# Performance work log

Hardware: AMD Instinct MI355X
Metric: run time of the kernel (lower is better)

Reference implementation:

```python
import jax, jax.numpy as jnp
import numpy as np


def setup_inputs() -> dict:
    key = jax.random.key(0)
    ks = jax.random.split(key, 10)
    B, C, D, H, W = 2, 512, 8, 32, 32
    Ck = C // 4  # shared KV head dim (and fixed query dim per intended MQA math)
    s = 0.02
    return {
        "x": jax.random.normal(ks[0], (B, C, D, H, W), dtype=jnp.float32),
        "Wq": jax.random.normal(ks[1], (Ck, C), dtype=jnp.float32) * s,
        "bq": jnp.zeros((Ck,), dtype=jnp.float32),
        "Wk": jax.random.normal(ks[2], (Ck, C), dtype=jnp.float32) * s,
        "bk": jnp.zeros((Ck,), dtype=jnp.float32),
        "Wv": jax.random.normal(ks[3], (Ck, C), dtype=jnp.float32) * s,
        "bv": jnp.zeros((Ck,), dtype=jnp.float32),
        "Wo": jax.random.normal(ks[4], (C, C), dtype=jnp.float32) * s,
        "bo": jnp.zeros((C,), dtype=jnp.float32),
    }


def reference(x, Wq, bq, Wk, bk, Wv, bv, Wo, bo):
    B, C, D, H, W = x.shape
    N = D * H * W
    Ck = Wk.shape[0]  # C // 4
    xf = x.reshape(B, C, N)  # flatten spatial dims -> sequence axis
    # 1x1 Conv3d == per-voxel linear projection over channels
    q = jnp.einsum('oc,bcn->bno', Wq, xf) + bq  # [B, N, Ck]
    k = jnp.einsum('oc,bcn->bno', Wk, xf) + bk  # [B, N, Ck]
    v = jnp.einsum('oc,bcn->bno', Wv, xf) + bv  # [B, N, Ck]
    scale = jnp.asarray(Ck, x.dtype) ** -0.5
    attn = jax.nn.softmax(jnp.einsum('bnc,bmc->bnm', q, k) * scale, axis=-1)  # [B, N, N]
    out = jnp.einsum('bnm,bmc->bnc', attn, v)  # [B, N, Ck]
    out = jnp.tile(out, (1, 1, 4))  # repeat(1,1,4) -> [B, N, C]
    out = jnp.einsum('oc,bnc->bon', Wo, out) + bo[None, :, None]  # [B, C, N]
    return out.reshape(B, C, D, H, W) + x
```

## Files before the change

kernel.cpp:

```cpp
#include <hip/hip_runtime.h>
#include <hip/hip_bf16.h>

typedef __bf16 bf16;
typedef __bf16 bf16x8 __attribute__((ext_vector_type(8)));
typedef __bf16 bf16x4 __attribute__((ext_vector_type(4)));
typedef float  f32x4  __attribute__((ext_vector_type(4)));
typedef float  f32x16 __attribute__((ext_vector_type(16)));
typedef unsigned int u32;
typedef u32 u32x4 __attribute__((ext_vector_type(4)));

constexpr int BB = 2, C = 512, NN = 8192, CK = 128;

__device__ __forceinline__ u32 cvt_pk_bf16(float lo, float hi) {
    u32 r;
    asm("v_cvt_pk_bf16_f32 %0, %1, %2" : "=v"(r) : "v"(lo), "v"(hi));
    return r;
}
__device__ __forceinline__ void pl32_swap(u32& a, u32& b) {
    asm("v_permlane32_swap_b32 %0, %1" : "+v"(a), "+v"(b));
}

__global__ __launch_bounds__(256) void k_qkv(
    const float* __restrict__ x,
    const float* __restrict__ Wq, const float* __restrict__ bq,
    const float* __restrict__ Wk, const float* __restrict__ bk,
    const float* __restrict__ Wv, const float* __restrict__ bv,
    bf16* __restrict__ qkv_ws)
{
    const int t = threadIdx.x;
    const int lane = t & 63, w = t >> 6;
    const int lr = lane & 15, lg = lane >> 4;
    const int n0 = blockIdx.x * 128;
    const int which = blockIdx.y;
    const int b = blockIdx.z;
    const float* W    = which == 0 ? Wq : (which == 1 ? Wk : Wv);
    const float* bias = which == 0 ? bq : (which == 1 ? bk : bv);
    bf16* out = qkv_ws + (size_t)which * BB * NN * CK;

    __shared__ __align__(16) char s_xT[128 * 144];
    __shared__ __align__(16) char s_w [128 * 144];

    f32x4 acc[2][8];
#pragma unroll
    for (int m = 0; m < 2; m++)
#pragma unroll
        for (int j = 0; j < 8; j++) acc[m][j] = (f32x4){0.f, 0.f, 0.f, 0.f};

    const float* xb = x + (size_t)b * C * NN;

    const int tok4 = (t & 31) * 4;
    const int c8   = (t >> 5) * 8;
    const int ob   = t >> 2;
    const int c16  = (t & 3) * 16;

    for (int kt = 0; kt < C; kt += 64) {
        __syncthreads();
        {
            float4 v[8];
#pragma unroll
            for (int i = 0; i < 8; i++)
                v[i] = *(const float4*)(xb + (size_t)(kt + c8 + i) * NN + n0 + tok4);
#pragma unroll
            for (int j = 0; j < 4; j++) {
                int tok = tok4 + j;
                bf16x8 pk = { (bf16)v[0].x, (bf16)v[1].x, (bf16)v[2].x, (bf16)v[3].x,
                              (bf16)v[4].x, (bf16)v[5].x, (bf16)v[6].x, (bf16)v[7].x };
                if (j == 1) pk = (bf16x8){ (bf16)v[0].y, (bf16)v[1].y, (bf16)v[2].y, (bf16)v[3].y,
                                           (bf16)v[4].y, (bf16)v[5].y, (bf16)v[6].y, (bf16)v[7].y };
                if (j == 2) pk = (bf16x8){ (bf16)v[0].z, (bf16)v[1].z, (bf16)v[2].z, (bf16)v[3].z,
                                           (bf16)v[4].z, (bf16)v[5].z, (bf16)v[6].z, (bf16)v[7].z };
                if (j == 3) pk = (bf16x8){ (bf16)v[0].w, (bf16)v[1].w, (bf16)v[2].w, (bf16)v[3].w,
                                           (bf16)v[4].w, (bf16)v[5].w, (bf16)v[6].w, (bf16)v[7].w };
                int off = tok * 144 + ((c8 * 2) ^ ((((tok >> 2) & 7)) << 4));
                *(bf16x8*)(s_xT + off) = pk;
            }
        }
#pragma unroll
        for (int p = 0; p < 2; p++) {
            int o = ob + p * 64;
            const float* wp = W + (size_t)o * C + kt + c16;
            float4 a0 = *(const float4*)(wp);
            float4 a1 = *(const float4*)(wp + 4);
            float4 a2 = *(const float4*)(wp + 8);
            float4 a3 = *(const float4*)(wp + 12);
            bf16x8 p0 = { (bf16)a0.x, (bf16)a0.y, (bf16)a0.z, (bf16)a0.w,
                          (bf16)a1.x, (bf16)a1.y, (bf16)a1.z, (bf16)a1.w };
            bf16x8 p1 = { (bf16)a2.x, (bf16)a2.y, (bf16)a2.z, (bf16)a2.w,
                          (bf16)a3.x, (bf16)a3.y, (bf16)a3.z, (bf16)a3.w };
            int perm = ((o >> 2) & 7) << 4;
            *(bf16x8*)(s_w + o * 144 + ((c16 * 2) ^ perm)) = p0;
            *(bf16x8*)(s_w + o * 144 + ((c16 * 2 + 16) ^ perm)) = p1;
        }
        __syncthreads();
#pragma unroll
        for (int ks = 0; ks < 2; ks++) {
            bf16x8 af[2];
#pragma unroll
            for (int m = 0; m < 2; m++) {
                int row = w * 32 + m * 16 + lr;
                af[m] = *(const bf16x8*)(s_xT + row * 144 + ((ks * 64 + lg * 16) ^ ((((row >> 2) & 7)) << 4)));
            }
#pragma unroll
            for (int j = 0; j < 8; j++) {
                int row = j * 16 + lr;
                bf16x8 bfr = *(const bf16x8*)(s_w + row * 144 + ((ks * 64 + lg * 16) ^ ((((row >> 2) & 7)) << 4)));
                acc[0][j] = __builtin_amdgcn_mfma_f32_16x16x32_bf16(af[0], bfr, acc[0][j], 0, 0, 0);
                acc[1][j] = __builtin_amdgcn_mfma_f32_16x16x32_bf16(af[1], bfr, acc[1][j], 0, 0, 0);
            }
        }
    }
#pragma unroll
    for (int m = 0; m < 2; m++)
#pragma unroll
        for (int j = 0; j < 8; j++) {
            int o = j * 16 + lr;
            float bia = bias[o];
#pragma unroll
            for (int r = 0; r < 4; r++) {
                int tok = n0 + w * 32 + m * 16 + lg * 4 + r;
                out[((size_t)b * NN + tok) * CK + o] = (bf16)(acc[m][j][r] + bia);
            }
        }
}

__global__ __launch_bounds__(512, 2) void k_attn(
    const bf16* __restrict__ qkv_ws,
    float* __restrict__ Opart, float* __restrict__ Lw,
    int nsplit)
{
    const int t = threadIdx.x;
    const int lane = t & 63, w = t >> 6;
    const int lq = lane & 31, hi = lane >> 5;

    const int total = 32 * BB * nsplit;
    const int chunkv = total >> 3;
    const int lin = blockIdx.x;
    const int rid = (lin & 7) * chunkv + (lin >> 3);
    const int qt = rid & 31;
    const int bs = rid >> 5;
    const int b = bs & 1, split = bs >> 1;

    const int q0 = qt * 256;
    const int kbeg = split * (NN / nsplit);
    const int nt = (NN / nsplit) / 64;

    const bf16* kg = qkv_ws + (size_t)BB * NN * CK;
    const bf16* vg = qkv_ws + (size_t)2 * BB * NN * CK;

    __shared__ __align__(16) char s_k[2][64 * 256];
    __shared__ __align__(16) char s_vt[3][128 * 128];

    const int kb0 = lq * 256 + ((((lq & 7) ^ hi)) << 4);
    int vbs[4];
#pragma unroll
    for (int db = 0; db < 4; db++) {
        int d = db * 32 + lq;
        vbs[db] = d * 128 + (((((d ^ (d >> 3)) & 7) ^ hi)) << 4);
    }
    const int t2 = t & 255;
    const int sc = t2 & 15, sr = t2 >> 4;
    const int kw_base = (sr * 256 + sc * 16) ^ ((sr & 7) << 4);
    const int vw_base = (sc * 1024 + sr * 8) ^ ((sc & 7) << 4);

    bf16x8 qf[8];
    {
        const float qs = 0.08838834764831845f * 1.4426950408889634f;
        const bf16* qp = qkv_ws + ((size_t)b * NN + q0 + w * 32 + lq) * CK + hi * 8;
#pragma unroll
        for (int ks = 0; ks < 8; ks++) {
            bf16x8 v = *(const bf16x8*)(qp + ks * 16);
#pragma unroll
            for (int i = 0; i < 8; i++) qf[ks][i] = (bf16)((float)v[i] * qs);
        }
    }

    f32x16 oacc[4];
#pragma unroll
    for (int db = 0; db < 4; db++)
#pragma unroll
        for (int i = 0; i < 16; i++) oacc[db][i] = 0.f;
    float lrun = 0.f;

    const bf16* kp = kg + ((size_t)b * NN + kbeg + sr) * CK + sc * 8;
    const bf16* vp = vg + ((size_t)b * NN + kbeg + sr * 4) * CK + sc * 8;
    bf16x8 stg[4];

    auto issue_loads = [&]() {
        if (w < 4) {
#pragma unroll
            for (int p = 0; p < 4; p++) stg[p] = *(const bf16x8*)(kp + (size_t)(16 * p) * CK);
        } else {
#pragma unroll
            for (int p = 0; p < 4; p++) stg[p] = *(const bf16x8*)(vp + (size_t)p * CK);
        }
        kp += (size_t)64 * CK;
        vp += (size_t)64 * CK;
    };

    auto write_lds = [&](int kbuf, int vbuf) {
        if (w < 4) {
            char* skw = s_k[kbuf] + kw_base;
#pragma unroll
            for (int p = 0; p < 4; p++)
                *(bf16x8*)(skw + p * 4096) = stg[p];
        } else {
            char* svw = s_vt[vbuf];
#pragma unroll
            for (int i = 0; i < 8; i++) {
                bf16x4 pk = { stg[0][i], stg[1][i], stg[2][i], stg[3][i] };
                *(bf16x4*)(svw + (vw_base ^ (i * 144))) = pk;
            }
        }
    };

    f32x16 sa0, sa1;
    auto do_qkt = [&](const char* sk) {
#pragma unroll
        for (int i = 0; i < 16; i++) { sa0[i] = 0.f; sa1[i] = 0.f; }
#pragma unroll
        for (int ks = 0; ks < 8; ks++) {
            bf16x8 kf0 = *(const bf16x8*)(sk + (kb0 ^ (ks * 32)));
            bf16x8 kf1 = *(const bf16x8*)(sk + ((kb0 ^ (ks * 32)) + 8192));
            sa0 = __builtin_amdgcn_mfma_f32_32x32x16_bf16(kf0, qf[ks], sa0, 0, 0, 0);
            sa1 = __builtin_amdgcn_mfma_f32_32x32x16_bf16(kf1, qf[ks], sa1, 0, 0, 0);
        }
    };

    u32 W0[8], W1[8];
    auto do_softmax = [&]() {
        f32x16 p0, p1;
#pragma unroll
        for (int i = 0; i < 16; i++) { p0[i] = exp2f(sa0[i]); p1[i] = exp2f(sa1[i]); }
        float s0 = ((p0[0] + p0[1]) + (p0[2] + p0[3])) + ((p0[4] + p0[5]) + (p0[6] + p0[7]));
        float s1 = ((p0[8] + p0[9]) + (p0[10] + p0[11])) + ((p0[12] + p0[13]) + (p0[14] + p0[15]));
        float s2 = ((p1[0] + p1[1]) + (p1[2] + p1[3])) + ((p1[4] + p1[5]) + (p1[6] + p1[7]));
        float s3 = ((p1[8] + p1[9]) + (p1[10] + p1[11])) + ((p1[12] + p1[13]) + (p1[14] + p1[15]));
        lrun += (s0 + s1) + (s2 + s3);
#pragma unroll
        for (int j = 0; j < 8; j++) {
            W0[j] = cvt_pk_bf16(p0[2 * j], p0[2 * j + 1]);
            W1[j] = cvt_pk_bf16(p1[2 * j], p1[2 * j + 1]);
        }
        pl32_swap(W0[0], W0[2]); pl32_swap(W0[1], W0[3]);
        pl32_swap(W0[4], W0[6]); pl32_swap(W0[5], W0[7]);
        pl32_swap(W1[0], W1[2]); pl32_swap(W1[1], W1[3]);
        pl32_swap(W1[4], W1[6]); pl32_swap(W1[5], W1[7]);
    };

    auto do_pv = [&](const char* sv) {
#pragma unroll
        for (int s = 0; s < 4; s++) {
            u32x4 fw;
            if (s == 0)      fw = (u32x4){W0[0], W0[1], W0[2], W0[3]};
            else if (s == 1) fw = (u32x4){W0[4], W0[5], W0[6], W0[7]};
            else if (s == 2) fw = (u32x4){W1[0], W1[1], W1[2], W1[3]};
            else             fw = (u32x4){W1[4], W1[5], W1[6], W1[7]};
            bf16x8 pa = __builtin_bit_cast(bf16x8, fw);
            const int coff = (s >> 1) * 64 + (s & 1) * 32;
#pragma unroll
            for (int db = 0; db < 4; db++) {
                bf16x8 vf = *(const bf16x8*)(sv + (vbs[db] ^ coff));
                oacc[db] = __builtin_amdgcn_mfma_f32_32x32x16_bf16(pa, vf, oacc[db], 0, 0, 0);
            }
        }
    };

    issue_loads();
    write_lds(0, 0);
    __syncthreads();
    if (nt > 1) issue_loads();
    __builtin_amdgcn_s_setprio(1);
    do_qkt(s_k[0]);
    __builtin_amdgcn_s_setprio(0);
    do_softmax();

    int vb_w = 1, vb_r = 0;
    for (int it = 1; it < nt; it++) {
        write_lds(it & 1, vb_w);
        __syncthreads();
        if (it + 1 < nt) issue_loads();
        __builtin_amdgcn_s_setprio(1);
        do_qkt(s_k[it & 1]);
        do_pv(s_vt[vb_r]);
        __builtin_amdgcn_s_setprio(0);
        do_softmax();
        vb_r = vb_w;
        vb_w = vb_w + 1 == 3 ? 0 : vb_w + 1;
    }
    __builtin_amdgcn_s_setprio(1);
    do_pv(s_vt[vb_r]);
    __builtin_amdgcn_s_setprio(0);

    size_t obase = (((size_t)split * BB + b) * NN + q0 + w * 32);
    float ls = lrun + __shfl_xor(lrun, 32);
    if (lane < 32) {
        Lw[obase + lq] = ls;
    }
#pragma unroll
    for (int r = 0; r < 16; r++) {
        int qrow = (r & 3) + 8 * (r >> 2) + 4 * hi;
        float* op = Opart + (obase + qrow) * CK + lq;
#pragma unroll
        for (int db = 0; db < 4; db++) op[db * 32] = oacc[db][r];
    }
}

__global__ __launch_bounds__(256) void k_combine(
    const float* __restrict__ Opart, const float* __restrict__ Lw,
    bf16* __restrict__ ao, int nsplit)
{
    const int t = threadIdx.x;
    const int b = blockIdx.y;
    const int r0 = blockIdx.x * 64;
    const int d4 = (t & 31) * 4;
#pragma unroll
    for (int p = 0; p < 8; p++) {
        int row = r0 + (t >> 5) + p * 8;
        size_t rbase = (size_t)b * NN + row;
        float L = 0.f;
        float4 acc = {0.f, 0.f, 0.f, 0.f};
        for (int s = 0; s < nsplit; s++) {
            size_t sb = ((size_t)s * BB) * NN + rbase;
            L += Lw[sb];
            float4 v = *(const float4*)(Opart + sb * CK + d4);
            acc.x += v.x; acc.y += v.y;
            acc.z += v.z; acc.w += v.w;
        }
        float inv = 1.f / L;
        bf16x4 o4 = { (bf16)(acc.x * inv), (bf16)(acc.y * inv),
                      (bf16)(acc.z * inv), (bf16)(acc.w * inv) };
        *(bf16x4*)(ao + rbase * CK + d4) = o4;
    }
}

__global__ __launch_bounds__(256) void k_out(
    const float* __restrict__ x, const float* __restrict__ Wo, const float* __restrict__ bo,
    const bf16* __restrict__ ao, float* __restrict__ y)
{
    const int t = threadIdx.x;
    const int lane = t & 63, w = t >> 6;
    const int lr = lane & 15, lg = lane >> 4;
    const int n0 = blockIdx.x * 128;
    const int o0 = blockIdx.y * 64;
    const int b = blockIdx.z;

    __shared__ __align__(16) char s_w[64 * 256];
    __shared__ __align__(16) char s_a[128 * 256];

    {
        int c4 = (t & 31) * 4, rbase = t >> 5;
#pragma unroll
        for (int p = 0; p < 8; p++) {
            int row = rbase + p * 8;
            const float* wp = Wo + (size_t)(o0 + row) * C + c4;
            float4 a0 = *(const float4*)(wp);
            float4 a1 = *(const float4*)(wp + 128);
            float4 a2 = *(const float4*)(wp + 256);
            float4 a3 = *(const float4*)(wp + 384);
            bf16x4 r4 = { (bf16)(a0.x + a1.x + a2.x + a3.x), (bf16)(a0.y + a1.y + a2.y + a3.y),
                          (bf16)(a0.z + a1.z + a2.z + a3.z), (bf16)(a0.w + a1.w + a2.w + a3.w) };
            int off = (row * 256 + c4 * 2) ^ ((row & 7) << 4);
            *(bf16x4*)(s_w + off) = r4;
        }
    }
    {
        int chunk = t & 15, rbase = t >> 4;
#pragma unroll
        for (int p = 0; p < 8; p++) {
            int row = rbase + p * 16;
            bf16x8 v = *(const bf16x8*)(ao + ((size_t)b * NN + n0 + row) * CK + chunk * 8);
            int off = (row * 256 + chunk * 16) ^ ((row & 7) << 4);
            *(bf16x8*)(s_a + off) = v;
        }
    }
    __syncthreads();

    f32x4 acc[8];
#pragma unroll
    for (int j = 0; j < 8; j++) acc[j] = (f32x4){0.f, 0.f, 0.f, 0.f};
#pragma unroll
    for (int ks = 0; ks < 4; ks++) {
        int row = w * 16 + lr;
        int aoff = (row * 256 + (ks * 32 + lg * 8) * 2) ^ ((row & 7) << 4);
        bf16x8 wf = *(const bf16x8*)(s_w + aoff);
#pragma unroll
        for (int j = 0; j < 8; j++) {
            int nrow = j * 16 + lr;
            int boff = (nrow * 256 + (ks * 32 + lg * 8) * 2) ^ ((nrow & 7) << 4);
            bf16x8 af = *(const bf16x8*)(s_a + boff);
            acc[j] = __builtin_amdgcn_mfma_f32_16x16x32_bf16(wf, af, acc[j], 0, 0, 0);
        }
    }
#pragma unroll
    for (int j = 0; j < 8; j++) {
        int n = n0 + j * 16 + lr;
#pragma unroll
        for (int r = 0; r < 4; r++) {
            int o = o0 + w * 16 + lg * 4 + r;
            size_t idx = ((size_t)b * C + o) * NN + n;
            y[idx] = acc[j][r] + bo[o] + x[idx];
        }
    }
}

extern "C" void kernel_launch(void* const* d_in, const int* in_sizes, int n_in,
                              void* d_out, int out_size, void* d_ws, size_t ws_size,
                              hipStream_t stream)
{
    const float* x  = (const float*)d_in[0];
    const float* Wq = (const float*)d_in[1];
    const float* bq = (const float*)d_in[2];
    const float* Wk = (const float*)d_in[3];
    const float* bk = (const float*)d_in[4];
    const float* Wv = (const float*)d_in[5];
    const float* bv = (const float*)d_in[6];
    const float* Wo = (const float*)d_in[7];
    const float* bo = (const float*)d_in[8];
    float* y = (float*)d_out;

    const size_t qkv_elems = (size_t)3 * BB * NN * CK;
    const size_t ao_elems  = (size_t)BB * NN * CK;

    bf16* qkv = (bf16*)d_ws;
    bf16* ao  = qkv + qkv_elems;
    float* Opart = (float*)(ao + ao_elems);

    int nsplit = 4;
    {
        size_t fixed = (qkv_elems + ao_elems) * sizeof(bf16);
        size_t per_split = ((size_t)BB * NN * CK + (size_t)BB * NN) * sizeof(float);
        while (nsplit > 1 && fixed + (size_t)nsplit * per_split > ws_size) nsplit >>= 1;
    }
    float* Lw = Opart + (size_t)nsplit * BB * NN * CK;

    k_qkv<<<dim3(NN / 128, 3, BB), 256, 0, stream>>>(x, Wq, bq, Wk, bk, Wv, bv, qkv);
    k_attn<<<dim3(32 * BB * nsplit, 1, 1), 512, 0, stream>>>(qkv, Opart, Lw, nsplit);
    k_combine<<<dim3(NN / 64, BB), 256, 0, stream>>>(Opart, Lw, ao, nsplit);
    k_out<<<dim3(NN / 128, C / 64, BB), 256, 0, stream>>>(x, Wo, bo, ao, y);
}
```

Baseline: 145.5 us.

## Enlarge attention blocks to 1024 threads, raise KV split, remap QKV grid

```diff
diff --git a/kernel.cpp b/kernel.cpp
--- a/kernel.cpp
+++ b/kernel.cpp
@@ -30,9 +30,14 @@
     const int t = threadIdx.x;
     const int lane = t & 63, w = t >> 6;
     const int lr = lane & 15, lg = lane >> 4;
-    const int n0 = blockIdx.x * 128;
-    const int which = blockIdx.y;
-    const int b = blockIdx.z;
+
+    const int lin = blockIdx.x;
+    const int rid = (lin & 7) * 48 + (lin >> 3);
+    const int n0 = (rid / 6) * 128;
+    const int sub = rid % 6;
+    const int which = sub >> 1;
+    const int b = sub & 1;
+
     const float* W    = which == 0 ? Wq : (which == 1 ? Wk : Wv);
     const float* bias = which == 0 ? bq : (which == 1 ? bk : bv);
     bf16* out = qkv_ws + (size_t)which * BB * NN * CK;
@@ -123,7 +128,7 @@
         }
 }
 
-__global__ __launch_bounds__(512, 2) void k_attn(
+__global__ __launch_bounds__(1024, 4) void k_attn(
     const bf16* __restrict__ qkv_ws,
     float* __restrict__ Opart, float* __restrict__ Lw,
     int nsplit)
@@ -132,15 +137,15 @@
     const int lane = t & 63, w = t >> 6;
     const int lq = lane & 31, hi = lane >> 5;
 
-    const int total = 32 * BB * nsplit;
+    const int total = 16 * BB * nsplit;
     const int chunkv = total >> 3;
     const int lin = blockIdx.x;
     const int rid = (lin & 7) * chunkv + (lin >> 3);
-    const int qt = rid & 31;
-    const int bs = rid >> 5;
+    const int qt = rid & 15;
+    const int bs = rid >> 4;
     const int b = bs & 1, split = bs >> 1;
 
-    const int q0 = qt * 256;
+    const int q0 = qt * 512;
     const int kbeg = split * (NN / nsplit);
     const int nt = (NN / nsplit) / 64;
 
@@ -157,10 +162,16 @@
         int d = db * 32 + lq;
         vbs[db] = d * 128 + (((((d ^ (d >> 3)) & 7) ^ hi)) << 4);
     }
-    const int t2 = t & 255;
-    const int sc = t2 & 15, sr = t2 >> 4;
-    const int kw_base = (sr * 256 + sc * 16) ^ ((sr & 7) << 4);
-    const int vw_base = (sc * 1024 + sr * 8) ^ ((sc & 7) << 4);
+    const int t2 = t & 511;
+    const int sck = t2 & 15, srk = t2 >> 4;
+    const int kw_base = (srk * 256 + sck * 16) ^ ((srk & 7) << 4);
+    const int sc4 = t2 & 31, sr4 = t2 >> 5;
+    int vw_addr[4];
+#pragma unroll
+    for (int i = 0; i < 4; i++) {
+        int d = sc4 * 4 + i;
+        vw_addr[i] = d * 128 + ((sr4 * 8) ^ (((d ^ (d >> 3)) & 7) << 4));
+    }
 
     bf16x8 qf[8];
     {
@@ -181,34 +192,35 @@
         for (int i = 0; i < 16; i++) oacc[db][i] = 0.f;
     float lrun = 0.f;
 
-    const bf16* kp = kg + ((size_t)b * NN + kbeg + sr) * CK + sc * 8;
-    const bf16* vp = vg + ((size_t)b * NN + kbeg + sr * 4) * CK + sc * 8;
-    bf16x8 stg[4];
+    const bf16* kp = kg + ((size_t)b * NN + kbeg + srk) * CK + sck * 8;
+    const bf16* vp = vg + ((size_t)b * NN + kbeg + sr4 * 4) * CK + sc4 * 4;
+    bf16x8 stgK[2];
+    bf16x4 stgV[4];
 
     auto issue_loads = [&]() {
-        if (w < 4) {
-#pragma unroll
-            for (int p = 0; p < 4; p++) stg[p] = *(const bf16x8*)(kp + (size_t)(16 * p) * CK);
+        if (w < 8) {
+#pragma unroll
+            for (int p = 0; p < 2; p++) stgK[p] = *(const bf16x8*)(kp + (size_t)(32 * p) * CK);
         } else {
 #pragma unroll
-            for (int p = 0; p < 4; p++) stg[p] = *(const bf16x8*)(vp + (size_t)p * CK);
+            for (int p = 0; p < 4; p++) stgV[p] = *(const bf16x4*)(vp + (size_t)p * CK);
         }
         kp += (size_t)64 * CK;
         vp += (size_t)64 * CK;
     };
 
     auto write_lds = [&](int kbuf, int vbuf) {
-        if (w < 4) {
+        if (w < 8) {
             char* skw = s_k[kbuf] + kw_base;
 #pragma unroll
-            for (int p = 0; p < 4; p++)
-                *(bf16x8*)(skw + p * 4096) = stg[p];
+            for (int p = 0; p < 2; p++)
+                *(bf16x8*)(skw + p * 8192) = stgK[p];
         } else {
             char* svw = s_vt[vbuf];
 #pragma unroll
-            for (int i = 0; i < 8; i++) {
-                bf16x4 pk = { stg[0][i], stg[1][i], stg[2][i], stg[3][i] };
-                *(bf16x4*)(svw + (vw_base ^ (i * 144))) = pk;
+            for (int i = 0; i < 4; i++) {
+                bf16x4 pk = { stgV[0][i], stgV[1][i], stgV[2][i], stgV[3][i] };
+                *(bf16x4*)(svw + vw_addr[i]) = pk;
             }
         }
     };
@@ -425,7 +437,7 @@
     bf16* ao  = qkv + qkv_elems;
     float* Opart = (float*)(ao + ao_elems);
 
-    int nsplit = 4;
+    int nsplit = 8;
     {
         size_t fixed = (qkv_elems + ao_elems) * sizeof(bf16);
         size_t per_split = ((size_t)BB * NN * CK + (size_t)BB * NN) * sizeof(float);
@@ -433,8 +445,8 @@
     }
     float* Lw = Opart + (size_t)nsplit * BB * NN * CK;
 
-    k_qkv<<<dim3(NN / 128, 3, BB), 256, 0, stream>>>(x, Wq, bq, Wk, bk, Wv, bv, qkv);
-    k_attn<<<dim3(32 * BB * nsplit, 1, 1), 512, 0, stream>>>(qkv, Opart, Lw, nsplit);
+    k_qkv<<<dim3(384, 1, 1), 256, 0, stream>>>(x, Wq, bq, Wk, bk, Wv, bv, qkv);
+    k_attn<<<dim3(16 * BB * nsplit, 1, 1), 1024, 0, stream>>>(qkv, Opart, Lw, nsplit);
     k_combine<<<dim3(NN / 64, BB), 256, 0, stream>>>(Opart, Lw, ao, nsplit);
     k_out<<<dim3(NN / 128, C / 64, BB), 256, 0, stream>>>(x, Wo, bo, ao, y);
 }
```

New measurement: 285.9 us. +96.5%, slower.
